# Kernel tuning notes

Hardware: AMD Instinct MI355X
Metric: run time of the kernel (lower is better)

## Reference

```python
import jax, jax.numpy as jnp
import numpy as np

B, T, D, H = 32, 512, 512, 1024


def setup_inputs() -> dict:
    key = jax.random.key(0)
    k1, k2, k3 = jax.random.split(key, 3)
    X = jax.random.normal(k1, (B, T, D), dtype=jnp.float32)
    # TF GRUCell variables: gates/kernel [D+H, 2H], gates/bias [2H] (init 1.0),
    # candidate/kernel [D+H, H], candidate/bias [H] (init 0.0). Use small random
    # values for a non-degenerate numerical baseline.
    gate_kernel = jax.random.normal(k2, (D + H, 2 * H), dtype=jnp.float32) * 0.02
    gate_bias = jnp.ones((2 * H,), dtype=jnp.float32)
    cand_kernel = jax.random.normal(k3, (D + H, H), dtype=jnp.float32) * 0.02
    cand_bias = jnp.zeros((H,), dtype=jnp.float32)
    return {"X": X, "gate_kernel": gate_kernel, "gate_bias": gate_bias,
            "cand_kernel": cand_kernel, "cand_bias": cand_bias}


def reference(X, gate_kernel, gate_bias, cand_kernel, cand_bias):
    """Static unidirectional GRU (TF GRUCell math), activation=tanh.
    Returns stacked per-step hidden states [B, T, H]; final state is out[:, -1]."""
    h0 = jnp.zeros((X.shape[0], cand_kernel.shape[1]), dtype=X.dtype)

    def step(h, x_t):
        # gates: r (reset), u (update) = sigmoid([x, h] @ Wg + bg)
        gates = jax.nn.sigmoid(jnp.concatenate([x_t, h], axis=-1) @ gate_kernel + gate_bias)
        r, u = jnp.split(gates, 2, axis=-1)
        # candidate: tanh([x, r*h] @ Wc + bc)
        c = jnp.tanh(jnp.concatenate([x_t, r * h], axis=-1) @ cand_kernel + cand_bias)
        h_new = u * h + (1.0 - u) * c
        return h_new, h_new

    _, hs = jax.lax.scan(step, h0, jnp.swapaxes(X, 0, 1))  # hs: [T, B, H]
    return jnp.swapaxes(hs, 0, 1)  # [B, T, H]
```

## Files before the change

kernel.cpp:

```cpp
#include <hip/hip_runtime.h>
#include <hip/hip_bf16.h>

typedef short s8v __attribute__((ext_vector_type(8)));
typedef float f4v __attribute__((ext_vector_type(4)));
typedef unsigned int u4v __attribute__((ext_vector_type(4)));
typedef unsigned int u2v __attribute__((ext_vector_type(2)));

#define NBLK 64
#define TPB 512

constexpr int BB = 32, TT = 512, DD = 512, HH = 1024;
constexpr int KK = DD + HH;
constexpr int PK = KK + 8;
constexpr int PK8 = PK / 8;
constexpr int K8 = KK / 8;

constexpr size_t OFF_WGT = 0;
constexpr size_t SZ_WGT  = (size_t)2 * HH * KK * 2;
constexpr size_t OFF_WCT = OFF_WGT + SZ_WGT;
constexpr size_t SZ_WCT  = (size_t)HH * KK * 2;
constexpr size_t OFF_XBF = OFF_WCT + SZ_WCT;
constexpr size_t SZ_XBF  = (size_t)BB * TT * DD * 2;
constexpr size_t OFF_HPB = OFF_XBF + SZ_XBF;
constexpr size_t SZ_PUB  = (size_t)BB * HH * 2;
constexpr size_t OFF_RPB = OFF_HPB + SZ_PUB;
constexpr size_t OFF_FLG = OFF_RPB + SZ_PUB;
constexpr size_t SZ_FLG  = (size_t)2 * NBLK * 8 * 4;

__global__ void wtr_kernel(const float* __restrict__ in, unsigned short* __restrict__ out, int N) {
    __shared__ float tl[32][33];
    int tx = threadIdx.x & 31, ty = threadIdx.x >> 5;
    int n0 = blockIdx.x * 32, k0 = blockIdx.y * 32;
#pragma unroll
    for (int r = ty; r < 32; r += 8) tl[r][tx] = in[(size_t)(k0 + r) * N + n0 + tx];
    __syncthreads();
#pragma unroll
    for (int r = ty; r < 32; r += 8) {
        __hip_bfloat16 h = __float2bfloat16(tl[tx][r]);
        out[(size_t)(n0 + r) * KK + k0 + tx] = *reinterpret_cast<unsigned short*>(&h);
    }
}

__global__ void xconv_kernel(const float* __restrict__ X, unsigned short* __restrict__ Xbf) {
    size_t i = ((size_t)blockIdx.x * 256 + threadIdx.x) * 4;
    float4 v = *reinterpret_cast<const float4*>(X + i);
    __hip_bfloat16 h0 = __float2bfloat16(v.x), h1 = __float2bfloat16(v.y);
    __hip_bfloat16 h2 = __float2bfloat16(v.z), h3 = __float2bfloat16(v.w);
    ushort4 o;
    o.x = *(unsigned short*)&h0; o.y = *(unsigned short*)&h1;
    o.z = *(unsigned short*)&h2; o.w = *(unsigned short*)&h3;
    *reinterpret_cast<ushort4*>(Xbf + i) = o;
}

__device__ __forceinline__ u4v cload16(const void* p) {
    u4v r; asm volatile("global_load_dwordx4 %0, %1, off sc0 sc1" : "=v"(r) : "v"(p) : "memory"); return r;
}
__device__ __forceinline__ void cstore8(void* p, u2v v) {
    asm volatile("global_store_dwordx2 %0, %1, off sc0 sc1" :: "v"(p), "v"(v) : "memory");
}
__device__ __forceinline__ void cstore4(void* p, int v) {
    asm volatile("global_store_dword %0, %1, off sc0 sc1" :: "v"(p), "v"(v) : "memory");
}
#define B16(x) __builtin_bit_cast(s8v, (x))
#define WAIT_VM(n) do { asm volatile("s_waitcnt vmcnt(" #n ")" ::: "memory"); \
                        __builtin_amdgcn_sched_barrier(0); } while (0)

__device__ __forceinline__ void pollq(const int* flags, int blk0, int rtw, int gen, int lane) {
    if (lane < 16) {
        const int* fp = flags + (size_t)(blk0 + lane) * 8 + rtw * 4;
        while (true) {
            u4v f; asm volatile("global_load_dwordx4 %0, %1, off sc0 sc1\ns_waitcnt vmcnt(0)"
                                : "=v"(f) : "v"(fp) : "memory");
            if ((int)f[0] >= gen && (int)f[1] >= gen && (int)f[2] >= gen && (int)f[3] >= gen) break;
            __builtin_amdgcn_s_sleep(1);
        }
    }
    asm volatile("" ::: "memory");
}

#define MFMA(A, B, C) __builtin_amdgcn_mfma_f32_16x16x32_bf16((A), (B), (C), 0, 0, 0)

__device__ __forceinline__ float bfu2f(unsigned short u) {
    unsigned int w = (unsigned int)u << 16;
    return __builtin_bit_cast(float, w);
}

__global__ __launch_bounds__(TPB, 1) void gru_kernel(
    const unsigned short* __restrict__ Xbf,
    const unsigned short* __restrict__ WgT,
    const unsigned short* __restrict__ WcT,
    const float* __restrict__ bg,
    const float* __restrict__ bc,
    float* __restrict__ out,
    unsigned short* __restrict__ hpub,
    unsigned short* __restrict__ rpub,
    int* __restrict__ gflagA,
    int* __restrict__ gflagB)
{
    __shared__ unsigned short sWg[32 * PK];
    __shared__ unsigned short sWc[16 * PK];
    __shared__ float sPrc[4][2][16][16];
    __shared__ unsigned short sPu[4][2][16][16];
    __shared__ unsigned short stage[8][4][16];

    const int b    = blockIdx.x;
    const int tid  = threadIdx.x;
    const int wid  = tid >> 6;
    const int lane = tid & 63;
    const int l15  = lane & 15;
    const int lq   = lane >> 4;
    const int ks   = wid >> 1;
    const int rt   = wid & 1;
    const int arow = rt * 16 + l15;
    const int bcol0= b * 16;
    const int finm = ks * 4 + (lane >> 4);
    const int finrow = rt * 16 + finm;
    const int fincol = bcol0 + l15;

    {
        s8v* dst = (s8v*)sWg;
        for (int idx = tid; idx < 32 * K8; idx += TPB) {
            int c = idx / K8, k8 = idx % K8;
            int gc = (c < 16) ? (bcol0 + c) : (HH + bcol0 + (c - 16));
            dst[c * PK8 + k8] = ((const s8v*)(WgT + (size_t)gc * KK))[k8];
        }
        s8v* dst2 = (s8v*)sWc;
        for (int idx = tid; idx < 16 * K8; idx += TPB) {
            int c = idx / K8, k8 = idx % K8;
            dst2[c * PK8 + k8] = ((const s8v*)(WcT + (size_t)(bcol0 + c) * KK))[k8];
        }
    }

    const float bgr = bg[fincol];
    const float bgu = bg[HH + fincol];
    const float bcv = bc[fincol];

    const s8v* sWg8 = (const s8v*)sWg;
    const s8v* sWc8 = (const s8v*)sWc;
    const s8v* bwr = sWg8 + l15 * PK8 + lq;
    const s8v* bwu = sWg8 + (16 + l15) * PK8 + lq;
    const s8v* bwc = sWc8 + l15 * PK8 + lq;
    const s8v* bwrx = bwr + 16 * ks;
    const s8v* bwux = bwu + 16 * ks;
    const s8v* bwrh = bwr + 64 + 32 * ks;
    const s8v* bwuh = bwu + 64 + 32 * ks;
    const s8v* bwcx = bwc + 16 * ks;
    const s8v* bwch = bwc + 64 + 32 * ks;

    float hprev = 0.f;

    __syncthreads();

#pragma unroll 1
    for (int t = 0; t < TT; ++t) {
        const s8v* xk = (const s8v*)(Xbf + (size_t)arow * (TT * DD) + (size_t)t * DD) + lq + 16 * ks;
        s8v x0 = xk[0], x1 = xk[4], x2 = xk[8], x3 = xk[12];

        f4v ar0 = {0,0,0,0}, ar1 = {0,0,0,0};
        ar0 = MFMA(x0, bwrx[0],  ar0); ar1 = MFMA(x1, bwrx[4],  ar1);
        ar0 = MFMA(x2, bwrx[8],  ar0); ar1 = MFMA(x3, bwrx[12], ar1);
        u4v hb[8];
        if (t > 0) {
            pollq(gflagB, ks * 16, rt, t, lane);
            const unsigned short* hp = hpub + (size_t)arow * HH + ks * 256 + lq * 8;
#pragma unroll
            for (int j = 0; j < 8; ++j) hb[j] = cload16(hp + (size_t)j * 32);
            WAIT_VM(4);
            ar0 = MFMA(B16(hb[0]), bwrh[0],  ar0); ar1 = MFMA(B16(hb[1]), bwrh[4],  ar1);
            ar0 = MFMA(B16(hb[2]), bwrh[8],  ar0); ar1 = MFMA(B16(hb[3]), bwrh[12], ar1);
            WAIT_VM(0);
            ar0 = MFMA(B16(hb[4]), bwrh[16], ar0); ar1 = MFMA(B16(hb[5]), bwrh[20], ar1);
            ar0 = MFMA(B16(hb[6]), bwrh[24], ar0); ar1 = MFMA(B16(hb[7]), bwrh[28], ar1);
        }
        f4v pr = ar0 + ar1;
#pragma unroll
        for (int i = 0; i < 4; ++i) sPrc[ks][rt][lq * 4 + i][l15] = pr[i];
        __syncthreads();

        {
            float zr = sPrc[0][rt][finm][l15] + sPrc[1][rt][finm][l15]
                     + sPrc[2][rt][finm][l15] + sPrc[3][rt][finm][l15] + bgr;
            float r = 1.f / (1.f + __expf(-zr));
            __hip_bfloat16 hb16 = __float2bfloat16(r * hprev);
            stage[wid][lane >> 4][l15] = *(unsigned short*)&hb16;
            if (t > 0) {
                if (lane < 16) {
                    u2v v = *reinterpret_cast<const u2v*>(&stage[wid][lane >> 2][(lane & 3) * 4]);
                    cstore8(rpub + (size_t)(rt * 16 + ks * 4 + (lane >> 2)) * HH + bcol0 + (lane & 3) * 4, v);
                }
                asm volatile("s_waitcnt vmcnt(0)" ::: "memory");
                if (lane == 0) cstore4(gflagA + b * 8 + rt * 4 + ks, t);
            }
        }

        f4v au0 = {0,0,0,0}, au1 = {0,0,0,0};
        au0 = MFMA(x0, bwux[0],  au0); au1 = MFMA(x1, bwux[4],  au1);
        au0 = MFMA(x2, bwux[8],  au0); au1 = MFMA(x3, bwux[12], au1);
        if (t > 0) {
            au0 = MFMA(B16(hb[0]), bwuh[0],  au0); au1 = MFMA(B16(hb[1]), bwuh[4],  au1);
            au0 = MFMA(B16(hb[2]), bwuh[8],  au0); au1 = MFMA(B16(hb[3]), bwuh[12], au1);
            au0 = MFMA(B16(hb[4]), bwuh[16], au0); au1 = MFMA(B16(hb[5]), bwuh[20], au1);
            au0 = MFMA(B16(hb[6]), bwuh[24], au0); au1 = MFMA(B16(hb[7]), bwuh[28], au1);
        }
        f4v pu = au0 + au1;
#pragma unroll
        for (int i = 0; i < 4; ++i) {
            __hip_bfloat16 ub = __float2bfloat16(pu[i]);
            sPu[ks][rt][lq * 4 + i][l15] = *(unsigned short*)&ub;
        }
        f4v c0 = {0,0,0,0}, c1 = {0,0,0,0};
        c0 = MFMA(x0, bwcx[0],  c0); c1 = MFMA(x1, bwcx[4],  c1);
        c0 = MFMA(x2, bwcx[8],  c0); c1 = MFMA(x3, bwcx[12], c1);
        __syncthreads();

        float ureg;
        {
            float zu = bfu2f(sPu[0][rt][finm][l15]) + bfu2f(sPu[1][rt][finm][l15])
                     + bfu2f(sPu[2][rt][finm][l15]) + bfu2f(sPu[3][rt][finm][l15]) + bgu;
            ureg = 1.f / (1.f + __expf(-zu));
        }

        if (t > 0) {
            pollq(gflagA, ks * 16, rt, t, lane);
            const unsigned short* rp = rpub + (size_t)arow * HH + ks * 256 + lq * 8;
            u4v rb[8];
#pragma unroll
            for (int j = 0; j < 8; ++j) rb[j] = cload16(rp + (size_t)j * 32);
            WAIT_VM(4);
            c0 = MFMA(B16(rb[0]), bwch[0],  c0); c1 = MFMA(B16(rb[1]), bwch[4],  c1);
            c0 = MFMA(B16(rb[2]), bwch[8],  c0); c1 = MFMA(B16(rb[3]), bwch[12], c1);
            WAIT_VM(0);
            c0 = MFMA(B16(rb[4]), bwch[16], c0); c1 = MFMA(B16(rb[5]), bwch[20], c1);
            c0 = MFMA(B16(rb[6]), bwch[24], c0); c1 = MFMA(B16(rb[7]), bwch[28], c1);
        }
        f4v pc = c0 + c1;
#pragma unroll
        for (int i = 0; i < 4; ++i) sPrc[ks][rt][lq * 4 + i][l15] = pc[i];
        __syncthreads();

        {
            float zc = sPrc[0][rt][finm][l15] + sPrc[1][rt][finm][l15]
                     + sPrc[2][rt][finm][l15] + sPrc[3][rt][finm][l15] + bcv;
            float e = __expf(2.f * zc);
            float cv = 1.f - 2.f / (e + 1.f);
            float hn = ureg * hprev + (1.f - ureg) * cv;
            hprev = hn;
            __hip_bfloat16 hb16 = __float2bfloat16(hn);
            stage[wid][lane >> 4][l15] = *(unsigned short*)&hb16;
            if (lane < 16) {
                u2v v = *reinterpret_cast<const u2v*>(&stage[wid][lane >> 2][(lane & 3) * 4]);
                cstore8(hpub + (size_t)(rt * 16 + ks * 4 + (lane >> 2)) * HH + bcol0 + (lane & 3) * 4, v);
            }
            asm volatile("s_waitcnt vmcnt(0)" ::: "memory");
            if (lane == 0) cstore4(gflagB + b * 8 + rt * 4 + ks, t + 1);
            out[(size_t)finrow * (TT * HH) + (size_t)t * HH + fincol] = hn;
        }
        __syncthreads();
    }
}

extern "C" void kernel_launch(void* const* d_in, const int* in_sizes, int n_in,
                              void* d_out, int out_size, void* d_ws, size_t ws_size,
                              hipStream_t stream) {
    const float* X  = (const float*)d_in[0];
    const float* gk = (const float*)d_in[1];
    const float* gb = (const float*)d_in[2];
    const float* ck = (const float*)d_in[3];
    const float* cb = (const float*)d_in[4];
    float* out = (float*)d_out;
    char* ws = (char*)d_ws;
    if (ws_size < OFF_FLG + SZ_FLG) return;

    unsigned short* WgT  = (unsigned short*)(ws + OFF_WGT);
    unsigned short* WcT  = (unsigned short*)(ws + OFF_WCT);
    unsigned short* Xbf  = (unsigned short*)(ws + OFF_XBF);
    unsigned short* hpub = (unsigned short*)(ws + OFF_HPB);
    unsigned short* rpub = (unsigned short*)(ws + OFF_RPB);
    int*            gflagA = (int*)(ws + OFF_FLG);
    int*            gflagB = gflagA + NBLK * 8;

    hipMemsetAsync(gflagA, 0, SZ_FLG, stream);

    dim3 tb(256);
    wtr_kernel<<<dim3(2 * HH / 32, KK / 32), tb, 0, stream>>>(gk, WgT, 2 * HH);
    wtr_kernel<<<dim3(HH / 32, KK / 32), tb, 0, stream>>>(ck, WcT, HH);
    xconv_kernel<<<(BB * TT * DD) / (256 * 4), tb, 0, stream>>>(X, Xbf);

    gru_kernel<<<NBLK, dim3(TPB), 0, stream>>>(Xbf, WgT, WcT, gb, cb, out,
                                               hpub, rpub, gflagA, gflagB);
}
```

Measured before the change: 4.113 ms.

## Split GRU block into role-specialized waves with LDS flags instead of barriers

Reorganizes the persistent GRU kernel from 8 waves that split the K dimension (with LDS reductions and block barriers) into 6 waves with fixed roles: reset gate, update gate and candidate. Each role wave handles the full K range for one 16-row tile. Roles hand off through LDS spin flags rather than __syncthreads, and the update-gate wave publishes an early flag so the candidate wave can start sooner. This removes the cross-wave partial-sum reductions and barriers from the per-step critical path. In exchange each wave runs a longer serial MFMA chain and issues more global loads, and correctness now depends on hand-written LDS and global flag ordering.

```diff
diff --git a/kernel.cpp b/kernel.cpp
--- a/kernel.cpp
+++ b/kernel.cpp
@@ -7,7 +7,7 @@
 typedef unsigned int u2v __attribute__((ext_vector_type(2)));
 
 #define NBLK 64
-#define TPB 512
+#define TPB 384
 
 constexpr int BB = 32, TT = 512, DD = 512, HH = 1024;
 constexpr int KK = DD + HH;
@@ -25,7 +25,7 @@
 constexpr size_t SZ_PUB  = (size_t)BB * HH * 2;
 constexpr size_t OFF_RPB = OFF_HPB + SZ_PUB;
 constexpr size_t OFF_FLG = OFF_RPB + SZ_PUB;
-constexpr size_t SZ_FLG  = (size_t)2 * NBLK * 8 * 4;
+constexpr size_t SZ_FLG  = (size_t)2 * NBLK * 4 * 4;
 
 __global__ void wtr_kernel(const float* __restrict__ in, unsigned short* __restrict__ out, int N) {
     __shared__ float tl[32][33];
@@ -65,25 +65,40 @@
 #define WAIT_VM(n) do { asm volatile("s_waitcnt vmcnt(" #n ")" ::: "memory"); \
                         __builtin_amdgcn_sched_barrier(0); } while (0)
 
-__device__ __forceinline__ void pollq(const int* flags, int blk0, int rtw, int gen, int lane) {
-    if (lane < 16) {
-        const int* fp = flags + (size_t)(blk0 + lane) * 8 + rtw * 4;
-        while (true) {
-            u4v f; asm volatile("global_load_dwordx4 %0, %1, off sc0 sc1\ns_waitcnt vmcnt(0)"
-                                : "=v"(f) : "v"(fp) : "memory");
-            if ((int)f[0] >= gen && (int)f[1] >= gen && (int)f[2] >= gen && (int)f[3] >= gen) break;
-            __builtin_amdgcn_s_sleep(1);
-        }
-    }
+__device__ __forceinline__ void poll1(const int* f, int gen, int lane) {
+    const int* fp = f + lane * 4;
+    while (__hip_atomic_load(fp, __ATOMIC_RELAXED, __HIP_MEMORY_SCOPE_AGENT) < gen)
+        __builtin_amdgcn_s_sleep(1);
     asm volatile("" ::: "memory");
 }
+__device__ __forceinline__ void poll2(const int* f, int gen, int lane) {
+    const int* fp = f + lane * 4;
+    while (true) {
+        u2v v; asm volatile("global_load_dwordx2 %0, %1, off sc0 sc1\ns_waitcnt vmcnt(0)"
+                            : "=v"(v) : "v"(fp) : "memory");
+        if ((int)v[0] >= gen && (int)v[1] >= gen) break;
+        __builtin_amdgcn_s_sleep(1);
+    }
+    asm volatile("" ::: "memory");
+}
+
+__device__ __forceinline__ void lds_spin(volatile int* p, int gen) {
+    while (*p < gen) __builtin_amdgcn_s_sleep(1);
+    asm volatile("s_waitcnt lgkmcnt(0)" ::: "memory");
+    __builtin_amdgcn_sched_barrier(0);
+}
+__device__ __forceinline__ void lds_set(volatile int* p, int gen, int lane) {
+    asm volatile("s_waitcnt lgkmcnt(0)" ::: "memory");
+    if (lane == 0) *p = gen;
+}
 
 #define MFMA(A, B, C) __builtin_amdgcn_mfma_f32_16x16x32_bf16((A), (B), (C), 0, 0, 0)
 
-__device__ __forceinline__ float bfu2f(unsigned short u) {
-    unsigned int w = (unsigned int)u << 16;
-    return __builtin_bit_cast(float, w);
-}
+#define C8(b0, r0, r1, r2, r3, r4, r5, r6, r7) \
+    a0 = MFMA(B16(r0), bwh[(b0 + 0) * 4], a0); a1 = MFMA(B16(r1), bwh[(b0 + 1) * 4], a1); \
+    a2 = MFMA(B16(r2), bwh[(b0 + 2) * 4], a2); a3 = MFMA(B16(r3), bwh[(b0 + 3) * 4], a3); \
+    a0 = MFMA(B16(r4), bwh[(b0 + 4) * 4], a0); a1 = MFMA(B16(r5), bwh[(b0 + 5) * 4], a1); \
+    a2 = MFMA(B16(r6), bwh[(b0 + 6) * 4], a2); a3 = MFMA(B16(r7), bwh[(b0 + 7) * 4], a3);
 
 __global__ __launch_bounds__(TPB, 1) void gru_kernel(
     const unsigned short* __restrict__ Xbf,
@@ -94,14 +109,15 @@
     float* __restrict__ out,
     unsigned short* __restrict__ hpub,
     unsigned short* __restrict__ rpub,
-    int* __restrict__ gflagA,
-    int* __restrict__ gflagB)
+    int* __restrict__ hflag,
+    int* __restrict__ fpair)
 {
     __shared__ unsigned short sWg[32 * PK];
     __shared__ unsigned short sWc[16 * PK];
-    __shared__ float sPrc[4][2][16][16];
-    __shared__ unsigned short sPu[4][2][16][16];
-    __shared__ unsigned short stage[8][4][16];
+    __shared__ float uLds[2][16][17];
+    __shared__ float hpLds[2][16][17];
+    __shared__ unsigned short stage[2][2][16][16];
+    __shared__ int lflag[2][2][16];
 
     const int b    = blockIdx.x;
     const int tid  = threadIdx.x;
@@ -109,13 +125,10 @@
     const int lane = tid & 63;
     const int l15  = lane & 15;
     const int lq   = lane >> 4;
-    const int ks   = wid >> 1;
     const int rt   = wid & 1;
+    const int role = wid >> 1;
     const int arow = rt * 16 + l15;
     const int bcol0= b * 16;
-    const int finm = ks * 4 + (lane >> 4);
-    const int finrow = rt * 16 + finm;
-    const int fincol = bcol0 + l15;
 
     {
         s8v* dst = (s8v*)sWg;
@@ -129,133 +142,115 @@
             int c = idx / K8, k8 = idx % K8;
             dst2[c * PK8 + k8] = ((const s8v*)(WcT + (size_t)(bcol0 + c) * KK))[k8];
         }
-    }
-
-    const float bgr = bg[fincol];
-    const float bgu = bg[HH + fincol];
-    const float bcv = bc[fincol];
+        if (tid < 4) lflag[tid >> 1][tid & 1][0] = 0;
+    }
 
     const s8v* sWg8 = (const s8v*)sWg;
     const s8v* sWc8 = (const s8v*)sWc;
-    const s8v* bwr = sWg8 + l15 * PK8 + lq;
-    const s8v* bwu = sWg8 + (16 + l15) * PK8 + lq;
-    const s8v* bwc = sWc8 + l15 * PK8 + lq;
-    const s8v* bwrx = bwr + 16 * ks;
-    const s8v* bwux = bwu + 16 * ks;
-    const s8v* bwrh = bwr + 64 + 32 * ks;
-    const s8v* bwuh = bwu + 64 + 32 * ks;
-    const s8v* bwcx = bwc + 16 * ks;
-    const s8v* bwch = bwc + 64 + 32 * ks;
-
-    float hprev = 0.f;
+    const s8v* bw = (role == 0) ? (sWg8 + l15 * PK8 + lq)
+                  : (role == 1) ? (sWg8 + (16 + l15) * PK8 + lq)
+                                : (sWc8 + l15 * PK8 + lq);
+    const s8v* bwx = bw;
+    const s8v* bwh = bw + DD / 8;
+    const float bias = (role == 0) ? bg[bcol0 + l15]
+                     : (role == 1) ? bg[HH + bcol0 + l15]
+                                   : bc[bcol0 + l15];
+
+    const unsigned short* srcbuf = (role == 2) ? rpub : hpub;
+    volatile int* myUflag  = &lflag[rt][0][0];
+    volatile int* myHpflag = &lflag[rt][1][0];
+
+    float hprevC[4] = {0.f, 0.f, 0.f, 0.f};
 
     __syncthreads();
 
 #pragma unroll 1
     for (int t = 0; t < TT; ++t) {
-        const s8v* xk = (const s8v*)(Xbf + (size_t)arow * (TT * DD) + (size_t)t * DD) + lq + 16 * ks;
-        s8v x0 = xk[0], x1 = xk[4], x2 = xk[8], x3 = xk[12];
-
-        f4v ar0 = {0,0,0,0}, ar1 = {0,0,0,0};
-        ar0 = MFMA(x0, bwrx[0],  ar0); ar1 = MFMA(x1, bwrx[4],  ar1);
-        ar0 = MFMA(x2, bwrx[8],  ar0); ar1 = MFMA(x3, bwrx[12], ar1);
-        u4v hb[8];
+        const s8v* xp = (const s8v*)(Xbf + (size_t)arow * (TT * DD) + (size_t)t * DD) + lq;
+
+        f4v a0 = {0,0,0,0}, a1 = {0,0,0,0}, a2 = {0,0,0,0}, a3 = {0,0,0,0};
+#pragma unroll
+        for (int c = 0; c < 16; c += 4) {
+            a0 = MFMA(xp[(c + 0) * 4], bwx[(c + 0) * 4], a0);
+            a1 = MFMA(xp[(c + 1) * 4], bwx[(c + 1) * 4], a1);
+            a2 = MFMA(xp[(c + 2) * 4], bwx[(c + 2) * 4], a2);
+            a3 = MFMA(xp[(c + 3) * 4], bwx[(c + 3) * 4], a3);
+        }
+
         if (t > 0) {
-            pollq(gflagB, ks * 16, rt, t, lane);
-            const unsigned short* hp = hpub + (size_t)arow * HH + ks * 256 + lq * 8;
-#pragma unroll
-            for (int j = 0; j < 8; ++j) hb[j] = cload16(hp + (size_t)j * 32);
-            WAIT_VM(4);
-            ar0 = MFMA(B16(hb[0]), bwrh[0],  ar0); ar1 = MFMA(B16(hb[1]), bwrh[4],  ar1);
-            ar0 = MFMA(B16(hb[2]), bwrh[8],  ar0); ar1 = MFMA(B16(hb[3]), bwrh[12], ar1);
+            if (role == 2) poll2(fpair, t, lane);
+            else           poll1(hflag, t, lane);
+            const unsigned short* src = srcbuf + (size_t)arow * HH + lq * 8;
+            u4v h0, h1, h2, h3, h4, h5, h6, h7, h8, h9, hA, hB, hC, hD, hE, hF;
+            h0 = cload16(src);       h1 = cload16(src + 32);  h2 = cload16(src + 64);  h3 = cload16(src + 96);
+            h4 = cload16(src + 128); h5 = cload16(src + 160); h6 = cload16(src + 192); h7 = cload16(src + 224);
+            h8 = cload16(src + 256); h9 = cload16(src + 288); hA = cload16(src + 320); hB = cload16(src + 352);
+            hC = cload16(src + 384); hD = cload16(src + 416); hE = cload16(src + 448); hF = cload16(src + 480);
+            WAIT_VM(8);
+            C8(0, h0, h1, h2, h3, h4, h5, h6, h7)
+            h0 = cload16(src + 512); h1 = cload16(src + 544); h2 = cload16(src + 576); h3 = cload16(src + 608);
+            h4 = cload16(src + 640); h5 = cload16(src + 672); h6 = cload16(src + 704); h7 = cload16(src + 736);
+            WAIT_VM(8);
+            C8(8, h8, h9, hA, hB, hC, hD, hE, hF)
+            h8 = cload16(src + 768); h9 = cload16(src + 800); hA = cload16(src + 832); hB = cload16(src + 864);
+            hC = cload16(src + 896); hD = cload16(src + 928); hE = cload16(src + 960); hF = cload16(src + 992);
+            WAIT_VM(8);
+            C8(16, h0, h1, h2, h3, h4, h5, h6, h7)
             WAIT_VM(0);
-            ar0 = MFMA(B16(hb[4]), bwrh[16], ar0); ar1 = MFMA(B16(hb[5]), bwrh[20], ar1);
-            ar0 = MFMA(B16(hb[6]), bwrh[24], ar0); ar1 = MFMA(B16(hb[7]), bwrh[28], ar1);
-        }
-        f4v pr = ar0 + ar1;
-#pragma unroll
-        for (int i = 0; i < 4; ++i) sPrc[ks][rt][lq * 4 + i][l15] = pr[i];
-        __syncthreads();
-
-        {
-            float zr = sPrc[0][rt][finm][l15] + sPrc[1][rt][finm][l15]
-                     + sPrc[2][rt][finm][l15] + sPrc[3][rt][finm][l15] + bgr;
-            float r = 1.f / (1.f + __expf(-zr));
-            __hip_bfloat16 hb16 = __float2bfloat16(r * hprev);
-            stage[wid][lane >> 4][l15] = *(unsigned short*)&hb16;
+            if (role == 1 && lane == 0) cstore4(fpair + b * 4 + 1, t);
+            C8(24, h8, h9, hA, hB, hC, hD, hE, hF)
+        }
+
+        float z[4];
+#pragma unroll
+        for (int i = 0; i < 4; ++i) z[i] = (a0[i] + a1[i]) + (a2[i] + a3[i]) + bias;
+
+        if (role == 0) {
             if (t > 0) {
-                if (lane < 16) {
-                    u2v v = *reinterpret_cast<const u2v*>(&stage[wid][lane >> 2][(lane & 3) * 4]);
-                    cstore8(rpub + (size_t)(rt * 16 + ks * 4 + (lane >> 2)) * HH + bcol0 + (lane & 3) * 4, v);
+                lds_spin(myHpflag, t);
+#pragma unroll
+                for (int i = 0; i < 4; ++i) {
+                    float r = 1.f / (1.f + __expf(-z[i]));
+                    float rh = r * hpLds[rt][lq * 4 + i][l15];
+                    __hip_bfloat16 hb16 = __float2bfloat16(rh);
+                    stage[rt][0][lq * 4 + i][l15] = *(unsigned short*)&hb16;
                 }
+                int prow = lane >> 2, pch = (lane & 3) * 4;
+                u2v v = *reinterpret_cast<const u2v*>(&stage[rt][0][prow][pch]);
+                cstore8(rpub + (size_t)(rt * 16 + prow) * HH + bcol0 + pch, v);
                 asm volatile("s_waitcnt vmcnt(0)" ::: "memory");
-                if (lane == 0) cstore4(gflagA + b * 8 + rt * 4 + ks, t);
+                if (lane == 0) cstore4(fpair + b * 4, t);
             }
-        }
-
-        f4v au0 = {0,0,0,0}, au1 = {0,0,0,0};
-        au0 = MFMA(x0, bwux[0],  au0); au1 = MFMA(x1, bwux[4],  au1);
-        au0 = MFMA(x2, bwux[8],  au0); au1 = MFMA(x3, bwux[12], au1);
-        if (t > 0) {
-            au0 = MFMA(B16(hb[0]), bwuh[0],  au0); au1 = MFMA(B16(hb[1]), bwuh[4],  au1);
-            au0 = MFMA(B16(hb[2]), bwuh[8],  au0); au1 = MFMA(B16(hb[3]), bwuh[12], au1);
-            au0 = MFMA(B16(hb[4]), bwuh[16], au0); au1 = MFMA(B16(hb[5]), bwuh[20], au1);
-            au0 = MFMA(B16(hb[6]), bwuh[24], au0); au1 = MFMA(B16(hb[7]), bwuh[28], au1);
-        }
-        f4v pu = au0 + au1;
-#pragma unroll
-        for (int i = 0; i < 4; ++i) {
-            __hip_bfloat16 ub = __float2bfloat16(pu[i]);
-            sPu[ks][rt][lq * 4 + i][l15] = *(unsigned short*)&ub;
-        }
-        f4v c0 = {0,0,0,0}, c1 = {0,0,0,0};
-        c0 = MFMA(x0, bwcx[0],  c0); c1 = MFMA(x1, bwcx[4],  c1);
-        c0 = MFMA(x2, bwcx[8],  c0); c1 = MFMA(x3, bwcx[12], c1);
-        __syncthreads();
-
-        float ureg;
-        {
-            float zu = bfu2f(sPu[0][rt][finm][l15]) + bfu2f(sPu[1][rt][finm][l15])
-                     + bfu2f(sPu[2][rt][finm][l15]) + bfu2f(sPu[3][rt][finm][l15]) + bgu;
-            ureg = 1.f / (1.f + __expf(-zu));
-        }
-
-        if (t > 0) {
-            pollq(gflagA, ks * 16, rt, t, lane);
-            const unsigned short* rp = rpub + (size_t)arow * HH + ks * 256 + lq * 8;
-            u4v rb[8];
-#pragma unroll
-            for (int j = 0; j < 8; ++j) rb[j] = cload16(rp + (size_t)j * 32);
-            WAIT_VM(4);
-            c0 = MFMA(B16(rb[0]), bwch[0],  c0); c1 = MFMA(B16(rb[1]), bwch[4],  c1);
-            c0 = MFMA(B16(rb[2]), bwch[8],  c0); c1 = MFMA(B16(rb[3]), bwch[12], c1);
-            WAIT_VM(0);
-            c0 = MFMA(B16(rb[4]), bwch[16], c0); c1 = MFMA(B16(rb[5]), bwch[20], c1);
-            c0 = MFMA(B16(rb[6]), bwch[24], c0); c1 = MFMA(B16(rb[7]), bwch[28], c1);
-        }
-        f4v pc = c0 + c1;
-#pragma unroll
-        for (int i = 0; i < 4; ++i) sPrc[ks][rt][lq * 4 + i][l15] = pc[i];
-        __syncthreads();
-
-        {
-            float zc = sPrc[0][rt][finm][l15] + sPrc[1][rt][finm][l15]
-                     + sPrc[2][rt][finm][l15] + sPrc[3][rt][finm][l15] + bcv;
-            float e = __expf(2.f * zc);
-            float cv = 1.f - 2.f / (e + 1.f);
-            float hn = ureg * hprev + (1.f - ureg) * cv;
-            hprev = hn;
-            __hip_bfloat16 hb16 = __float2bfloat16(hn);
-            stage[wid][lane >> 4][l15] = *(unsigned short*)&hb16;
-            if (lane < 16) {
-                u2v v = *reinterpret_cast<const u2v*>(&stage[wid][lane >> 2][(lane & 3) * 4]);
-                cstore8(hpub + (size_t)(rt * 16 + ks * 4 + (lane >> 2)) * HH + bcol0 + (lane & 3) * 4, v);
+        } else if (role == 1) {
+#pragma unroll
+            for (int i = 0; i < 4; ++i)
+                uLds[rt][lq * 4 + i][l15] = 1.f / (1.f + __expf(-z[i]));
+            lds_set(myUflag, t + 1, lane);
+        } else {
+            lds_spin(myUflag, t + 1);
+            float hn[4];
+#pragma unroll
+            for (int i = 0; i < 4; ++i) {
+                float e = __expf(2.f * z[i]);
+                float cv = 1.f - 2.f / (e + 1.f);
+                float u = uLds[rt][lq * 4 + i][l15];
+                hn[i] = u * hprevC[i] + (1.f - u) * cv;
+                hprevC[i] = hn[i];
+                __hip_bfloat16 hb16 = __float2bfloat16(hn[i]);
+                stage[rt][1][lq * 4 + i][l15] = *(unsigned short*)&hb16;
             }
+            int prow = lane >> 2, pch = (lane & 3) * 4;
+            u2v v = *reinterpret_cast<const u2v*>(&stage[rt][1][prow][pch]);
+            cstore8(hpub + (size_t)(rt * 16 + prow) * HH + bcol0 + pch, v);
             asm volatile("s_waitcnt vmcnt(0)" ::: "memory");
-            if (lane == 0) cstore4(gflagB + b * 8 + rt * 4 + ks, t + 1);
-            out[(size_t)finrow * (TT * HH) + (size_t)t * HH + fincol] = hn;
-        }
-        __syncthreads();
+            if (lane == 0) cstore4(hflag + b * 4, t + 1);
+#pragma unroll
+            for (int i = 0; i < 4; ++i) hpLds[rt][lq * 4 + i][l15] = hn[i];
+            lds_set(myHpflag, t + 1, lane);
+#pragma unroll
+            for (int i = 0; i < 4; ++i)
+                out[(size_t)(rt * 16 + lq * 4 + i) * (TT * HH) + (size_t)t * HH + bcol0 + l15] = hn[i];
+        }
     }
 }
 
@@ -276,10 +271,10 @@
     unsigned short* Xbf  = (unsigned short*)(ws + OFF_XBF);
     unsigned short* hpub = (unsigned short*)(ws + OFF_HPB);
     unsigned short* rpub = (unsigned short*)(ws + OFF_RPB);
-    int*            gflagA = (int*)(ws + OFF_FLG);
-    int*            gflagB = gflagA + NBLK * 8;
-
-    hipMemsetAsync(gflagA, 0, SZ_FLG, stream);
+    int*            hflag = (int*)(ws + OFF_FLG);
+    int*            fpair = hflag + NBLK * 4;
+
+    hipMemsetAsync(hflag, 0, SZ_FLG, stream);
 
     dim3 tb(256);
     wtr_kernel<<<dim3(2 * HH / 32, KK / 32), tb, 0, stream>>>(gk, WgT, 2 * HH);
@@ -287,5 +282,5 @@
     xconv_kernel<<<(BB * TT * DD) / (256 * 4), tb, 0, stream>>>(X, Xbf);
 
     gru_kernel<<<NBLK, dim3(TPB), 0, stream>>>(Xbf, WgT, WcT, gb, cb, out,
-                                               hpub, rpub, gflagA, gflagB);
-}
+                                               hpub, rpub, hflag, fpair);
+}
```

Measured after the change: 6.672 ms. +62.2%, slower.
